# Performance work log

Hardware: AMD Instinct MI355X
Metric: run time of the kernel (lower is better)

Reference implementation:

```python
import jax, jax.numpy as jnp
import numpy as np

B, H, W, C = 32, 56, 56, 192
WS, SHIFT, NH = 7, 3, 6
HD = C // NH
N = WS * WS
NW = (H // WS) * (W // WS)
SCALE = HD ** -0.5
EPS = 1e-5


def _layer_norm(x, g, b):
    mu = jnp.mean(x, axis=-1, keepdims=True)
    var = jnp.mean(jnp.square(x - mu), axis=-1, keepdims=True)
    return (x - mu) * jax.lax.rsqrt(var + EPS) * g + b


def _relative_position_index():
    coords = np.stack(np.meshgrid(np.arange(WS), np.arange(WS), indexing='ij'))  # [2,ws,ws]
    coords = coords.reshape(2, -1)                                               # [2,N]
    rel = coords[:, :, None] - coords[:, None, :]                                # [2,N,N]
    rel = rel.transpose(1, 2, 0).astype(np.int64)
    rel[..., 0] += WS - 1
    rel[..., 1] += WS - 1
    rel[..., 0] *= 2 * WS - 1
    return jnp.asarray(rel.sum(-1))  # [N,N]


def _attn_mask():
    img = np.zeros((H, W), dtype=np.float32)
    cnt = 0
    slices = (slice(0, -WS), slice(-WS, -SHIFT), slice(-SHIFT, None))
    for hs in slices:
        for ws_ in slices:
            img[hs, ws_] = cnt
            cnt += 1
    mw = img.reshape(H // WS, WS, W // WS, WS).transpose(0, 2, 1, 3).reshape(-1, N)  # [nW,N]
    diff = mw[:, :, None] - mw[:, None, :]
    return jnp.asarray(np.where(diff != 0, -100.0, 0.0).astype(np.float32))  # [nW,N,N]


REL_IDX = _relative_position_index()
ATTN_MASK = _attn_mask()


def setup_inputs() -> dict:
    key = jax.random.key(0)
    ks = jax.random.split(key, 16)
    s = 0.02
    return {
        'x': jax.random.normal(ks[0], (B, H * W, C), jnp.float32),
        'ln1_g': jnp.ones((C,), jnp.float32),
        'ln1_b': jnp.zeros((C,), jnp.float32),
        'qkv_w': jax.random.normal(ks[1], (3 * C, C), jnp.float32) * s,
        'qkv_b': jnp.zeros((3 * C,), jnp.float32),
        'proj_w': jax.random.normal(ks[2], (C, C), jnp.float32) * s,
        'proj_b': jnp.zeros((C,), jnp.float32),
        'rpb_table': jax.random.normal(ks[3], ((2 * WS - 1) ** 2, NH), jnp.float32) * s,
        'ln2_g': jnp.ones((C,), jnp.float32),
        'ln2_b': jnp.zeros((C,), jnp.float32),
        'fc1_w': jax.random.normal(ks[4], (4 * C, C), jnp.float32) * s,
        'fc1_b': jnp.zeros((4 * C,), jnp.float32),
        'fc2_w': jax.random.normal(ks[5], (C, 4 * C), jnp.float32) * s,
        'fc2_b': jnp.zeros((C,), jnp.float32),
    }


def reference(x, ln1_g, ln1_b, qkv_w, qkv_b, proj_w, proj_b, rpb_table,
              ln2_g, ln2_b, fc1_w, fc1_b, fc2_w, fc2_b):
    shortcut = x
    h = _layer_norm(x, ln1_g, ln1_b).reshape(B, H, W, C)
    # cyclic shift
    h = jnp.roll(h, (-SHIFT, -SHIFT), axis=(1, 2))
    # window partition -> [B*nW, N, C]
    h = h.reshape(B, H // WS, WS, W // WS, WS, C).transpose(0, 1, 3, 2, 4, 5)
    h = h.reshape(B * NW, N, C)
    # qkv
    qkv = h @ qkv_w.T + qkv_b                                   # [Bn,N,3C]
    qkv = qkv.reshape(B * NW, N, 3, NH, HD).transpose(2, 0, 3, 1, 4)
    q, k, v = qkv[0], qkv[1], qkv[2]                             # [Bn,nh,N,hd]
    attn = jnp.einsum('bhnd,bhmd->bhnm', q * SCALE, k)           # [Bn,nh,N,N]
    # relative position bias
    bias = rpb_table[REL_IDX.reshape(-1)].reshape(N, N, NH).transpose(2, 0, 1)
    attn = attn + bias[None]
    # shift mask
    attn = attn.reshape(B, NW, NH, N, N) + ATTN_MASK[None, :, None]
    attn = jax.nn.softmax(attn.reshape(B * NW, NH, N, N), axis=-1)
    h = jnp.einsum('bhnm,bhmd->bhnd', attn, v)                   # [Bn,nh,N,hd]
    h = h.transpose(0, 2, 1, 3).reshape(B * NW, N, C)
    h = h @ proj_w.T + proj_b
    # window reverse + reverse shift
    h = h.reshape(B, H // WS, W // WS, WS, WS, C).transpose(0, 1, 3, 2, 4, 5)
    h = h.reshape(B, H, W, C)
    h = jnp.roll(h, (SHIFT, SHIFT), axis=(1, 2)).reshape(B, H * W, C)
    x = shortcut + h
    # MLP
    m = _layer_norm(x, ln2_g, ln2_b)
    m = jax.nn.gelu(m @ fc1_w.T + fc1_b, approximate=False)
    m = m @ fc2_w.T + fc2_b
    return x + m
```

## Files before the change

kernel.cpp:

```cpp
#include <hip/hip_runtime.h>
#include <hip/hip_bf16.h>
#include <cstdint>
#include <cstddef>

typedef __hip_bfloat16 bf16;
using f32x4  = __attribute__((ext_vector_type(4))) float;
using bf16x8 = __attribute__((ext_vector_type(8))) short;

#define DEVI __device__ __forceinline__

DEVI int reg3(int u) { return (u < 49) ? 0 : ((u < 53) ? 1 : 2); }

DEVI unsigned short f2bu(float v) {
  bf16 b = __float2bfloat16(v);
  return *reinterpret_cast<unsigned short*>(&b);
}

DEVI float gelu_f(float v) {
  const float y = 0.7978845608028654f * (v + 0.044715f * v * v * v);
  const float e = __expf(2.0f * y);
  const float th = 1.0f - 2.0f / (e + 1.0f);
  return 0.5f * v * (1.0f + th);
}

DEVI void gload_lds16(const void* g, void* l) {
  __builtin_amdgcn_global_load_lds(
      (const __attribute__((address_space(1))) unsigned int*)g,
      (__attribute__((address_space(3))) unsigned int*)l, 16, 0, 0);
}

__global__ __launch_bounds__(256) void cvt_kernel(const float* __restrict__ src,
                                                  bf16* __restrict__ dst, int n)
{
  const int i = blockIdx.x * 256 + threadIdx.x;
  if (i < n) dst[i] = __float2bfloat16(src[i]);
}

template<bool PERM>
__global__ __launch_bounds__(256) void ln_kernel(const float* __restrict__ x,
                                                 const float* __restrict__ gw,
                                                 const float* __restrict__ bw,
                                                 bf16* __restrict__ out,
                                                 int grow0)
{
  const int lane = threadIdx.x & 63;
  const int ridx = blockIdx.x * 4 + (threadIdx.x >> 6);
  size_t src;
  if (PERM) {
    const int g   = grow0 + ridx;
    const int wid = g / 49;
    const int nn  = g - wid * 49;
    const int b_  = wid >> 6, wim = wid & 63;
    const int wy  = wim >> 3, wx = wim & 7;
    const int ny  = nn / 7,  nx = nn - (nn / 7) * 7;
    int i = wy * 7 + ny + 3; if (i >= 56) i -= 56;
    int j = wx * 7 + nx + 3; if (j >= 56) j -= 56;
    src = (size_t)(b_ * 3136 + i * 56 + j);
  } else {
    src = (size_t)ridx;
  }
  const float* xr = x + src * 192;
  float v0 = xr[lane];
  float v1 = xr[lane + 64];
  float v2 = xr[lane + 128];
  float s = v0 + v1 + v2;
#pragma unroll
  for (int off = 32; off > 0; off >>= 1) s += __shfl_xor(s, off);
  const float mu = s * (1.0f / 192.0f);
  const float d0 = v0 - mu, d1 = v1 - mu, d2 = v2 - mu;
  float vs = d0 * d0 + d1 * d1 + d2 * d2;
#pragma unroll
  for (int off = 32; off > 0; off >>= 1) vs += __shfl_xor(vs, off);
  const float rstd = rsqrtf(vs * (1.0f / 192.0f) + 1e-5f);
  bf16* orow = out + (size_t)ridx * 192;
  orow[lane]       = __float2bfloat16(d0 * rstd * gw[lane]       + bw[lane]);
  orow[lane + 64]  = __float2bfloat16(d1 * rstd * gw[lane + 64]  + bw[lane + 64]);
  orow[lane + 128] = __float2bfloat16(d2 * rstd * gw[lane + 128] + bw[lane + 128]);
}

template<int MODE>
__global__ __launch_bounds__(256) void gemm_kernel(const bf16* __restrict__ A,
                                                   const bf16* __restrict__ Bt,
                                                   const float* __restrict__ bias,
                                                   const float* __restrict__ resid,
                                                   void* __restrict__ outv,
                                                   int N, int K, int grow0)
{
  __shared__ short lds[2][128 * 64 + 192 * 64];
  const int tid  = threadIdx.x;
  const int lane = tid & 63;
  const int w    = tid >> 6;
  const int wm   = (w >> 1) * 64;
  const int wn   = (w & 1) * 96;
  const int m0   = blockIdx.y * 128;
  const int n0   = blockIdx.x * 192;
  const int lrow = lane >> 3;
  const int lseg = lane & 7;
  const int ksw  = (lseg * 8) ^ (lrow << 3);

  f32x4 acc[4][6];
#pragma unroll
  for (int i = 0; i < 4; i++)
#pragma unroll
    for (int j = 0; j < 6; j++) acc[i][j] = (f32x4){0.f, 0.f, 0.f, 0.f};

  const int nk = K >> 6;

  auto issue = [&](int buf, int kt) {
    const int k0 = kt << 6;
    short* LA = &lds[buf][0];
    short* LB = &lds[buf][128 * 64];
#pragma unroll
    for (int i = 0; i < 4; i++) {
      const int chunk = w * 4 + i;
      gload_lds16(A + (size_t)(m0 + chunk * 8 + lrow) * K + (k0 + ksw), LA + chunk * 512);
    }
#pragma unroll
    for (int i = 0; i < 6; i++) {
      const int chunk = w * 6 + i;
      gload_lds16(Bt + (size_t)(n0 + chunk * 8 + lrow) * K + (k0 + ksw), LB + chunk * 512);
    }
  };

  issue(0, 0);
  __syncthreads();

  for (int kt = 0; kt < nk; kt++) {
    const int buf = kt & 1;
    if (kt + 1 < nk) issue(buf ^ 1, kt + 1);
    const char* LA = (const char*)&lds[buf][0];
    const char* LB = (const char*)&lds[buf][128 * 64];
#pragma unroll
    for (int kk = 0; kk < 2; kk++) {
      bf16x8 af[4], bg[6];
#pragma unroll
      for (int mf = 0; mf < 4; mf++) {
        const int row = wm + mf * 16 + (lane & 15);
        const int kb  = (kk * 64 + ((lane >> 4) << 4)) ^ ((row & 7) << 4);
        af[mf] = *(const bf16x8*)(LA + row * 128 + kb);
      }
#pragma unroll
      for (int nf = 0; nf < 6; nf++) {
        const int row = wn + nf * 16 + (lane & 15);
        const int kb  = (kk * 64 + ((lane >> 4) << 4)) ^ ((row & 7) << 4);
        bg[nf] = *(const bf16x8*)(LB + row * 128 + kb);
      }
#pragma unroll
      for (int mf = 0; mf < 4; mf++)
#pragma unroll
        for (int nf = 0; nf < 6; nf++)
          acc[mf][nf] = __builtin_amdgcn_mfma_f32_16x16x32_bf16(af[mf], bg[nf], acc[mf][nf], 0, 0, 0);
    }
    __syncthreads();
  }

  float bv[6];
  int ncol[6];
#pragma unroll
  for (int nf = 0; nf < 6; nf++) {
    ncol[nf] = n0 + wn + nf * 16 + (lane & 15);
    bv[nf]   = bias[ncol[nf]];
  }
#pragma unroll
  for (int mf = 0; mf < 4; mf++) {
#pragma unroll
    for (int r = 0; r < 4; r++) {
      const int m = m0 + wm + mf * 16 + ((lane >> 4) << 2) + r;
      if constexpr (MODE == 1) {
        const int gm  = grow0 + m;
        const int wid = gm / 49;
        const int nn  = gm - wid * 49;
        const int b_  = wid >> 6, wim = wid & 63;
        const int wy  = wim >> 3, wx = wim & 7;
        const int ny  = nn / 7, nx = nn - (nn / 7) * 7;
        int i = wy * 7 + ny + 3; if (i >= 56) i -= 56;
        int j = wx * 7 + nx + 3; if (j >= 56) j -= 56;
        const size_t t = (size_t)(b_ * 3136 + i * 56 + j) * 192;
        float* O = (float*)outv;
#pragma unroll
        for (int nf = 0; nf < 6; nf++)
          O[t + ncol[nf]] = acc[mf][nf][r] + bv[nf] + resid[t + ncol[nf]];
      } else if constexpr (MODE == 3) {
        float* O = (float*)outv + (size_t)m * N;
#pragma unroll
        for (int nf = 0; nf < 6; nf++)
          O[ncol[nf]] = acc[mf][nf][r] + bv[nf] + O[ncol[nf]];
      } else {
        bf16* O = (bf16*)outv + (size_t)m * N;
#pragma unroll
        for (int nf = 0; nf < 6; nf++) {
          float v = acc[mf][nf][r] + bv[nf];
          if constexpr (MODE == 2) v = gelu_f(v);
          O[ncol[nf]] = __float2bfloat16(v);
        }
      }
    }
  }
}

__global__ __launch_bounds__(64) void attn_kernel(const bf16* __restrict__ qkv,
                                                  const float* __restrict__ rpb,
                                                  bf16* __restrict__ aout)
{
  __shared__ unsigned short Vt[32 * 64];
  __shared__ unsigned short Pl[64 * 64];
  __shared__ float Bl[169];
  const int lane = threadIdx.x;
  const int wid  = blockIdx.x;
  const int h    = blockIdx.y;
  const unsigned short* qkvu = (const unsigned short*)qkv;
  const size_t base = (size_t)wid * 49 * 576 + h * 32;

#pragma unroll
  for (int i = 0; i < 3; i++) {
    const int idx = lane + 64 * i;
    if (idx < 169) Bl[idx] = rpb[idx * 6 + h];
  }
#pragma unroll
  for (int i = 0; i < 8; i++)
    ((unsigned long long*)Vt)[lane + 64 * i] = 0ull;

#pragma unroll
  for (int it = 0; it < 7; it++) {
    const int idx = lane + 64 * it;
    if (idx < 392) {
      const int n  = idx >> 3;
      const int d0 = (idx & 7) * 4;
      ushort4 v = *(const ushort4*)(qkvu + base + (size_t)n * 576 + 384 + d0);
      Vt[(d0 + 0) * 64 + (n ^ (((d0 + 0) & 7) << 3))] = v.x;
      Vt[(d0 + 1) * 64 + (n ^ (((d0 + 1) & 7) << 3))] = v.y;
      Vt[(d0 + 2) * 64 + (n ^ (((d0 + 2) & 7) << 3))] = v.z;
      Vt[(d0 + 3) * 64 + (n ^ (((d0 + 3) & 7) << 3))] = v.w;
    }
  }

  bf16x8 qf[4], kf[4];
#pragma unroll
  for (int t = 0; t < 4; t++) {
    int rq = (lane & 15) + t * 16; if (rq > 48) rq = 48;
    qf[t] = *(const bf16x8*)(qkvu + base + (size_t)rq * 576 + ((lane >> 4) * 8));
    kf[t] = *(const bf16x8*)(qkvu + base + (size_t)rq * 576 + 192 + ((lane >> 4) * 8));
  }

  f32x4 s[4][4];
#pragma unroll
  for (int mt = 0; mt < 4; mt++)
#pragma unroll
    for (int nt = 0; nt < 4; nt++)
      s[mt][nt] = __builtin_amdgcn_mfma_f32_16x16x32_bf16(qf[mt], kf[nt],
                    (f32x4){0.f, 0.f, 0.f, 0.f}, 0, 0, 0);

  const int wim = wid & 63;
  const int wy = wim >> 3, wx = wim & 7;
  int labn[4], ch[4], cw[4];
  bool cval[4];
#pragma unroll
  for (int nt = 0; nt < 4; nt++) {
    const int C = (lane & 15) + nt * 16;
    cval[nt] = (C < 49);
    const int cc = cval[nt] ? C : 48;
    ch[nt] = cc / 7; cw[nt] = cc - ch[nt] * 7;
    labn[nt] = reg3(wy * 7 + ch[nt]) * 3 + reg3(wx * 7 + cw[nt]);
  }

#pragma unroll
  for (int mt = 0; mt < 4; mt++) {
    f32x4 rm, sm, inv;
#pragma unroll
    for (int r = 0; r < 4; r++) {
      int R = mt * 16 + ((lane >> 4) << 2) + r; if (R > 48) R = 48;
      const int mh = R / 7, mw = R - (R / 7) * 7;
      const int labm = reg3(wy * 7 + mh) * 3 + reg3(wx * 7 + mw);
#pragma unroll
      for (int nt = 0; nt < 4; nt++) {
        float sv = s[mt][nt][r] * 0.1767766953f
                 + Bl[(mh - ch[nt] + 6) * 13 + (mw - cw[nt] + 6)];
        if (labn[nt] != labm) sv -= 100.f;
        if (!cval[nt]) sv = -3e38f;
        s[mt][nt][r] = sv;
      }
      rm[r] = fmaxf(fmaxf(s[mt][0][r], s[mt][1][r]), fmaxf(s[mt][2][r], s[mt][3][r]));
    }
#pragma unroll
    for (int mk = 1; mk < 16; mk <<= 1)
#pragma unroll
      for (int r = 0; r < 4; r++) rm[r] = fmaxf(rm[r], __shfl_xor(rm[r], mk));
#pragma unroll
    for (int r = 0; r < 4; r++) {
      float acc = 0.f;
#pragma unroll
      for (int nt = 0; nt < 4; nt++) {
        const float p = __expf(s[mt][nt][r] - rm[r]);
        s[mt][nt][r] = p;
        acc += p;
      }
      sm[r] = acc;
    }
#pragma unroll
    for (int mk = 1; mk < 16; mk <<= 1)
#pragma unroll
      for (int r = 0; r < 4; r++) sm[r] += __shfl_xor(sm[r], mk);
#pragma unroll
    for (int r = 0; r < 4; r++) inv[r] = 1.0f / sm[r];
#pragma unroll
    for (int nt = 0; nt < 4; nt++)
#pragma unroll
      for (int r = 0; r < 4; r++) {
        const int R = mt * 16 + ((lane >> 4) << 2) + r;
        const int C = (lane & 15) + nt * 16;
        Pl[R * 64 + (C ^ ((R & 7) << 3))] = f2bu(s[mt][nt][r] * inv[r]);
      }
  }

  f32x4 o[4][2];
#pragma unroll
  for (int mt = 0; mt < 4; mt++)
#pragma unroll
    for (int n2 = 0; n2 < 2; n2++) o[mt][n2] = (f32x4){0.f, 0.f, 0.f, 0.f};
#pragma unroll
  for (int kk = 0; kk < 2; kk++) {
    const int kb = kk * 64 + ((lane >> 4) << 4);
    bf16x8 vb[2];
#pragma unroll
    for (int n2 = 0; n2 < 2; n2++) {
      const int d = (lane & 15) + n2 * 16;
      vb[n2] = *(const bf16x8*)((const char*)Vt + d * 128 + (kb ^ ((d & 7) << 4)));
    }
#pragma unroll
    for (int mt = 0; mt < 4; mt++) {
      const int R = (lane & 15) + mt * 16;
      const bf16x8 pa = *(const bf16x8*)((const char*)Pl + R * 128 + (kb ^ ((R & 7) << 4)));
#pragma unroll
      for (int n2 = 0; n2 < 2; n2++)
        o[mt][n2] = __builtin_amdgcn_mfma_f32_16x16x32_bf16(pa, vb[n2], o[mt][n2], 0, 0, 0);
    }
  }

#pragma unroll
  for (int mt = 0; mt < 4; mt++)
#pragma unroll
    for (int r = 0; r < 4; r++) {
      const int R = mt * 16 + ((lane >> 4) << 2) + r;
      if (R < 49) {
        bf16* orow = aout + (size_t)(wid * 49 + R) * 192 + h * 32;
#pragma unroll
        for (int n2 = 0; n2 < 2; n2++)
          orow[n2 * 16 + (lane & 15)] = __float2bfloat16(o[mt][n2][r]);
      }
    }
}

extern "C" void kernel_launch(void* const* d_in, const int* in_sizes, int n_in,
                              void* d_out, int out_size, void* d_ws, size_t ws_size,
                              hipStream_t stream)
{
  (void)in_sizes; (void)n_in; (void)out_size;
  const float* x     = (const float*)d_in[0];
  const float* ln1g  = (const float*)d_in[1];
  const float* ln1b  = (const float*)d_in[2];
  const float* qkvw  = (const float*)d_in[3];
  const float* qkvb  = (const float*)d_in[4];
  const float* projw = (const float*)d_in[5];
  const float* projb = (const float*)d_in[6];
  const float* rpb   = (const float*)d_in[7];
  const float* ln2g  = (const float*)d_in[8];
  const float* ln2b  = (const float*)d_in[9];
  const float* fc1w  = (const float*)d_in[10];
  const float* fc1b  = (const float*)d_in[11];
  const float* fc2w  = (const float*)d_in[12];
  const float* fc2b  = (const float*)d_in[13];
  float* out = (float*)d_out;
  char* ws   = (char*)d_ws;

  bf16* wqkv = (bf16*)(ws);
  bf16* wproj = (bf16*)(ws + 221184);
  bf16* wfc1 = (bf16*)(ws + 294912);
  bf16* wfc2 = (bf16*)(ws + 589824);
  cvt_kernel<<<dim3(432), dim3(256), 0, stream>>>(qkvw, wqkv, 110592);
  cvt_kernel<<<dim3(144), dim3(256), 0, stream>>>(projw, wproj, 36864);
  cvt_kernel<<<dim3(576), dim3(256), 0, stream>>>(fc1w, wfc1, 147456);
  cvt_kernel<<<dim3(576), dim3(256), 0, stream>>>(fc2w, wfc2, 147456);

  char* cws = ws + 884736;
  const size_t avail = (ws_size > 884736ull) ? ws_size - 884736ull : 0;

  int Bc = 32;
  while (Bc > 2 && (size_t)Bc * 4816896ull > avail) Bc >>= 1;
  const int nb = 32 / Bc;
  bf16* qkv_c  = (bf16*)cws;
  bf16* hwin_c = (bf16*)(cws + (size_t)Bc * 3612672ull);

  for (int c = 0; c < nb; c++) {
    const int R0 = c * Bc * 3136;
    const int Mc = Bc * 3136;
    ln_kernel<true><<<dim3(Mc / 4), dim3(256), 0, stream>>>(x, ln1g, ln1b, hwin_c, R0);
    gemm_kernel<0><<<dim3(3, Mc / 128), dim3(256), 0, stream>>>(hwin_c, wqkv, qkvb, nullptr, qkv_c, 576, 192, 0);
    attn_kernel<<<dim3(Bc * 64, 6), dim3(64), 0, stream>>>(qkv_c, rpb, hwin_c);
    gemm_kernel<1><<<dim3(1, Mc / 128), dim3(256), 0, stream>>>(hwin_c, wproj, projb, x, out, 192, 192, R0);
  }

  int Rc = 100352;
  while (Rc > 6272 && (size_t)Rc * 1920ull > avail) Rc >>= 1;
  bf16* ln2_c = (bf16*)cws;
  bf16* a1_c  = (bf16*)(cws + (size_t)Rc * 384ull);

  for (int r0 = 0; r0 < 100352; r0 += Rc) {
    ln_kernel<false><<<dim3(Rc / 4), dim3(256), 0, stream>>>(out + (size_t)r0 * 192, ln2g, ln2b, ln2_c, 0);
    gemm_kernel<2><<<dim3(4, Rc / 128), dim3(256), 0, stream>>>(ln2_c, wfc1, fc1b, nullptr, a1_c, 768, 192, 0);
    gemm_kernel<3><<<dim3(1, Rc / 128), dim3(256), 0, stream>>>(a1_c, wfc2, fc2b, nullptr, out + (size_t)r0 * 192, 192, 768, 0);
  }
}
```

Measured before the change: 374.0 us.

## Fuse LN2, FC1+GELU and FC2+residual into one MLP kernel

Replaces the three-kernel MLP path (layernorm, fc1 GEMM with GELU, fc2 GEMM with residual) with a single kernel. Each 32-row tile computes LN2, then the 768-wide hidden activation, which stays in swizzled shared memory, then fc2 plus residual. This removes the global round-trips for the LN output and the large bf16 hidden activation, plus two launches per chunk. In exchange, weights are read straight from global memory without LDS staging, and every block reloads the full fc1 and fc2 weights, which may be cache-bound.

```diff
diff --git a/kernel.cpp b/kernel.cpp
--- a/kernel.cpp
+++ b/kernel.cpp
@@ -180,21 +180,119 @@
 #pragma unroll
         for (int nf = 0; nf < 6; nf++)
           O[t + ncol[nf]] = acc[mf][nf][r] + bv[nf] + resid[t + ncol[nf]];
-      } else if constexpr (MODE == 3) {
-        float* O = (float*)outv + (size_t)m * N;
-#pragma unroll
-        for (int nf = 0; nf < 6; nf++)
-          O[ncol[nf]] = acc[mf][nf][r] + bv[nf] + O[ncol[nf]];
       } else {
         bf16* O = (bf16*)outv + (size_t)m * N;
 #pragma unroll
-        for (int nf = 0; nf < 6; nf++) {
-          float v = acc[mf][nf][r] + bv[nf];
-          if constexpr (MODE == 2) v = gelu_f(v);
-          O[ncol[nf]] = __float2bfloat16(v);
-        }
-      }
-    }
+        for (int nf = 0; nf < 6; nf++)
+          O[ncol[nf]] = __float2bfloat16(acc[mf][nf][r] + bv[nf]);
+      }
+    }
+  }
+}
+
+__global__ __launch_bounds__(512, 4) void mlp_kernel(const float* __restrict__ x,
+                                                     const float* __restrict__ g2,
+                                                     const float* __restrict__ b2,
+                                                     const bf16* __restrict__ w1,
+                                                     const float* __restrict__ b1f,
+                                                     const bf16* __restrict__ w2,
+                                                     const float* __restrict__ b2f,
+                                                     float* __restrict__ out)
+{
+  __shared__ char a0[32 * 384];
+  __shared__ char a1[32 * 1536];
+  const int tid  = threadIdx.x;
+  const int lane = tid & 63;
+  const int w    = tid >> 6;
+  const int m0   = blockIdx.x * 32;
+
+#pragma unroll
+  for (int i = 0; i < 4; i++) {
+    const int r = w * 4 + i;
+    const float* xr = x + (size_t)(m0 + r) * 192;
+    float v0 = xr[lane], v1 = xr[lane + 64], v2 = xr[lane + 128];
+    float s = v0 + v1 + v2;
+#pragma unroll
+    for (int off = 32; off > 0; off >>= 1) s += __shfl_xor(s, off);
+    const float mu = s * (1.0f / 192.0f);
+    const float d0 = v0 - mu, d1 = v1 - mu, d2 = v2 - mu;
+    float vs = d0 * d0 + d1 * d1 + d2 * d2;
+#pragma unroll
+    for (int off = 32; off > 0; off >>= 1) vs += __shfl_xor(vs, off);
+    const float rstd = rsqrtf(vs * (1.0f / 192.0f) + 1e-5f);
+    const int rx = (r & 7) << 4;
+    *(unsigned short*)(a0 + r * 384 + ((2 * lane) ^ rx))         = f2bu(d0 * rstd * g2[lane]       + b2[lane]);
+    *(unsigned short*)(a0 + r * 384 + ((2 * (lane + 64)) ^ rx))  = f2bu(d1 * rstd * g2[lane + 64]  + b2[lane + 64]);
+    *(unsigned short*)(a0 + r * 384 + ((2 * (lane + 128)) ^ rx)) = f2bu(d2 * rstd * g2[lane + 128] + b2[lane + 128]);
+  }
+  __syncthreads();
+
+  const int wm  = (w >> 2) * 16;
+  const int wn1 = (w & 3) * 192;
+  const int ar  = wm + (lane & 15);
+  const int arx = (ar & 7) << 4;
+  const int kq  = (lane >> 4);
+
+  f32x4 acc1[12];
+#pragma unroll
+  for (int j = 0; j < 12; j++) acc1[j] = (f32x4){0.f, 0.f, 0.f, 0.f};
+  for (int kk = 0; kk < 6; kk++) {
+    const bf16x8 af = *(const bf16x8*)(a0 + ar * 384 + ((kk * 64 + (kq << 4)) ^ arx));
+    const int kel = kk * 32 + (kq << 3);
+#pragma unroll
+    for (int h = 0; h < 2; h++) {
+      bf16x8 bf_[6];
+#pragma unroll
+      for (int nf = 0; nf < 6; nf++)
+        bf_[nf] = *(const bf16x8*)(w1 + (size_t)(wn1 + (h * 6 + nf) * 16 + (lane & 15)) * 192 + kel);
+#pragma unroll
+      for (int nf = 0; nf < 6; nf++)
+        acc1[h * 6 + nf] = __builtin_amdgcn_mfma_f32_16x16x32_bf16(af, bf_[nf], acc1[h * 6 + nf], 0, 0, 0);
+    }
+  }
+  {
+    float bv[12];
+#pragma unroll
+    for (int nf = 0; nf < 12; nf++) bv[nf] = b1f[wn1 + nf * 16 + (lane & 15)];
+#pragma unroll
+    for (int nf = 0; nf < 12; nf++)
+#pragma unroll
+      for (int r = 0; r < 4; r++) {
+        const int row = wm + (kq << 2) + r;
+        const int col = wn1 + nf * 16 + (lane & 15);
+        *(unsigned short*)(a1 + row * 1536 + ((2 * col) ^ ((row & 7) << 4)))
+            = f2bu(gelu_f(acc1[nf][r] + bv[nf]));
+      }
+  }
+  __syncthreads();
+
+  const int wn2 = (w & 3) * 48;
+  f32x4 acc2[3];
+#pragma unroll
+  for (int j = 0; j < 3; j++) acc2[j] = (f32x4){0.f, 0.f, 0.f, 0.f};
+  for (int kk = 0; kk < 24; kk++) {
+    const bf16x8 af = *(const bf16x8*)(a1 + ar * 1536 + ((kk * 64 + (kq << 4)) ^ arx));
+    const int kel = kk * 32 + (kq << 3);
+    bf16x8 bf_[3];
+#pragma unroll
+    for (int nf = 0; nf < 3; nf++)
+      bf_[nf] = *(const bf16x8*)(w2 + (size_t)(wn2 + nf * 16 + (lane & 15)) * 768 + kel);
+#pragma unroll
+    for (int nf = 0; nf < 3; nf++)
+      acc2[nf] = __builtin_amdgcn_mfma_f32_16x16x32_bf16(af, bf_[nf], acc2[nf], 0, 0, 0);
+  }
+  {
+    float bv[3];
+#pragma unroll
+    for (int nf = 0; nf < 3; nf++) bv[nf] = b2f[wn2 + nf * 16 + (lane & 15)];
+#pragma unroll
+    for (int nf = 0; nf < 3; nf++)
+#pragma unroll
+      for (int r = 0; r < 4; r++) {
+        const int row = wm + (kq << 2) + r;
+        const size_t o = (size_t)(m0 + row) * 192 + wn2 + nf * 16 + (lane & 15);
+        out[o] = acc2[nf][r] + bv[nf] + out[o];
+      }
   }
 }
 
@@ -399,14 +497,5 @@
     gemm_kernel<1><<<dim3(1, Mc / 128), dim3(256), 0, stream>>>(hwin_c, wproj, projb, x, out, 192, 192, R0);
   }
 
-  int Rc = 100352;
-  while (Rc > 6272 && (size_t)Rc * 1920ull > avail) Rc >>= 1;
-  bf16* ln2_c = (bf16*)cws;
-  bf16* a1_c  = (bf16*)(cws + (size_t)Rc * 384ull);
-
-  for (int r0 = 0; r0 < 100352; r0 += Rc) {
-    ln_kernel<false><<<dim3(Rc / 4), dim3(256), 0, stream>>>(out + (size_t)r0 * 192, ln2g, ln2b, ln2_c, 0);
-    gemm_kernel<2><<<dim3(4, Rc / 128), dim3(256), 0, stream>>>(ln2_c, wfc1, fc1b, nullptr, a1_c, 768, 192, 0);
-    gemm_kernel<3><<<dim3(1, Rc / 128), dim3(256), 0, stream>>>(a1_c, wfc2, fc2b, nullptr, out + (size_t)r0 * 192, 192, 768, 0);
-  }
-}
+  mlp_kernel<<<dim3(3136), dim3(512), 0, stream>>>(out, ln2g, ln2b, wfc1, fc1b, wfc2, fc2b, out);
+}
```

Result: slower. 632.0 us (+69.0%).
